# Performance work log

Hardware: AMD Instinct MI355X
Metric: run time of the kernel (lower is better)

Reference implementation:

```python
import jax, jax.numpy as jnp
import numpy as np

N = 100000   # total nodes in batch
E = 1200000  # total edges
D = 64       # dim_features (== hidden_dim)
H = 64       # hidden_dim
T = 32       # dim_targets
L = 3        # num_layers
G = 500      # number of graphs in batch


def setup_inputs() -> dict:
    key = jax.random.key(0)
    ks = jax.random.split(key, 16)
    s = 0.1
    inp = {
        "x": jax.random.normal(ks[0], (N, D), jnp.float32),
        "src": jax.random.randint(ks[1], (E,), 0, N, jnp.int32),
        "dst": jax.random.randint(ks[2], (E,), 0, N, jnp.int32),
        "graph_ids": jnp.sort(jax.random.randint(ks[3], (N,), 0, G, jnp.int32)),
        # GINConv learnable eps (init 0)
        "eps": jnp.zeros((L,), jnp.float32),
        # per-layer conv apply MLP: Linear(D->H), ReLU, Linear(H->H)
        "conv_w1": jax.random.normal(ks[4], (L, D, H), jnp.float32) * s,
        "conv_b1": jnp.zeros((L, H), jnp.float32),
        "conv_w2": jax.random.normal(ks[5], (L, H, H), jnp.float32) * s,
        "conv_b2": jnp.zeros((L, H), jnp.float32),
        # GraphNorm params
        "gn_weight": jnp.ones((L, H), jnp.float32),
        "gn_bias": jnp.zeros((L, H), jnp.float32),
        "gn_scale": jnp.ones((L, H), jnp.float32),
        # per-layer projection MLP: Linear(H->H), ReLU, Linear(H->T)
        "proj_w1": jax.random.normal(ks[6], (L, H, H), jnp.float32) * s,
        "proj_b1": jnp.zeros((L, H), jnp.float32),
        "proj_w2": jax.random.normal(ks[7], (L, H, T), jnp.float32) * s,
        "proj_b2": jnp.zeros((L, T), jnp.float32),
    }
    return inp


def reference(x, src, dst, graph_ids, eps, conv_w1, conv_b1, conv_w2, conv_b2,
              gn_weight, gn_bias, gn_scale, proj_w1, proj_b1, proj_w2, proj_b2):
    gid = graph_ids
    counts = jax.ops.segment_sum(jnp.ones((N,), x.dtype), gid, num_segments=G)
    safe = jnp.maximum(counts, 1.0)[:, None]  # [G,1] nodes per graph

    feat = x
    outs = []
    for l in range(L):
        # GINConv: (1+eps)*h_i + sum over incoming neighbors
        agg = jax.ops.segment_sum(feat[src], dst, num_segments=N)
        h = (1.0 + eps[l]) * feat + agg
        h = jnp.maximum(h @ conv_w1[l] + conv_b1[l], 0.0) @ conv_w2[l] + conv_b2[l]
        # GraphNorm: per-graph mean/std
        mean = jax.ops.segment_sum(h, gid, num_segments=G) / safe
        sub = h - mean[gid] * gn_scale[l]
        var = jax.ops.segment_sum(sub * sub, gid, num_segments=G) / safe
        std = jnp.sqrt(var + 1e-8)
        h = gn_weight[l] * sub / std[gid] + gn_bias[l]
        feat = jnp.maximum(h, 0.0)
        # projection MLP + per-graph mean pooling
        z = jnp.maximum(feat @ proj_w1[l] + proj_b1[l], 0.0) @ proj_w2[l] + proj_b2[l]
        outs.append(jax.ops.segment_sum(z, gid, num_segments=G) / safe)
    return jnp.concatenate(outs, axis=-1)  # [G, L*T]
```

## Files before the change

kernel.cpp:

```cpp
#include <hip/hip_runtime.h>
#include <math.h>

#define N_NODES 100000
#define N_EDGES 1200000
#define DIM 64
#define TDIM 32
#define NLAYERS 3
#define NGRAPH 500
#define NP (N_NODES + 1)

#define BUCKW 512
#define NBUCK ((N_NODES + BUCKW - 1) / BUCKW)
#define ECHUNK ((N_EDGES + 255) / 256)
#define MLPBL ((N_NODES + 63) / 64)

typedef unsigned short bfu;
typedef __attribute__((ext_vector_type(8))) short short8;
typedef __attribute__((ext_vector_type(4))) float v4f;

__device__ __forceinline__ float bf2f(bfu u) {
    union { unsigned int i; float f; } v; v.i = ((unsigned int)u) << 16; return v.f;
}
__device__ __forceinline__ float bflo(unsigned int d) {
    union { unsigned int i; float f; } v; v.i = d << 16; return v.f;
}
__device__ __forceinline__ float bfhi(unsigned int d) {
    union { unsigned int i; float f; } v; v.i = d & 0xFFFF0000u; return v.f;
}
__device__ __forceinline__ bfu f2bf(float f) {
    union { float f; unsigned int i; } v; v.f = f;
    unsigned int r = v.i + 0x7FFFu + ((v.i >> 16) & 1u);
    return (bfu)(r >> 16);
}

__global__ __launch_bounds__(256) void k_setup(const float* __restrict__ x, bfu* __restrict__ xb,
                                               const int* __restrict__ gid, int* __restrict__ gstart,
                                               float* __restrict__ inv_safe, float* __restrict__ ncnt,
                                               const float* __restrict__ w1, const float* __restrict__ w2,
                                               const float* __restrict__ q1, const float* __restrict__ q2,
                                               bfu* __restrict__ w1t, bfu* __restrict__ w2t,
                                               bfu* __restrict__ q1t, bfu* __restrict__ q2t,
                                               const int* __restrict__ dst, int* __restrict__ bcnt) {
    int b = blockIdx.x, t = threadIdx.x;
    if (b < 6250) {
        int base = (b * 256 + t) * 4;
        float4 v = *(const float4*)&x[base];
        ushort4 o;
        o.x = f2bf(v.x); o.y = f2bf(v.y); o.z = f2bf(v.z); o.w = f2bf(v.w);
        *(ushort4*)&xb[base] = o;
    } else if (b == 6250) {
        for (int tt = t; tt <= NGRAPH; tt += 256) {
            int lo = 0, hi = N_NODES;
            while (lo < hi) {
                int mid = (lo + hi) >> 1;
                if (gid[mid] < tt) lo = mid + 1; else hi = mid;
            }
            gstart[tt] = lo;
        }
        __syncthreads();
        for (int tt = t; tt < NGRAPH; tt += 256) {
            int c = gstart[tt + 1] - gstart[tt];
            inv_safe[tt] = 1.0f / (float)(c > 1 ? c : 1);
            ncnt[tt] = (float)c;
        }
    } else if (b < 6299) {
        int i = (b - 6251) * 256 + t;
        int l = i >> 12, k = (i >> 6) & 63, n = i & 63;
        int o = (l << 12) | (n << 6) | k;
        w1t[o] = f2bf(w1[i]);
        w2t[o] = f2bf(w2[i]);
        q1t[o] = f2bf(q1[i]);
        if (i < NLAYERS * 2048) {
            int l2 = i >> 11, rem = i & 2047, k2 = rem >> 5, n2 = rem & 31;
            q2t[l2 * 2048 + n2 * 64 + k2] = f2bf(q2[i]);
        }
    } else {
        __shared__ int h[NBUCK];
        for (int i = t; i < NBUCK; i += 256) h[i] = 0;
        __syncthreads();
        int e0 = (b - 6299) * ECHUNK;
        int e1 = e0 + ECHUNK; if (e1 > N_EDGES) e1 = N_EDGES;
        for (int e = e0 + t; e < e1; e += 256) atomicAdd(&h[dst[e] >> 9], 1);
        __syncthreads();
        for (int i = t; i < NBUCK; i += 256) if (h[i]) atomicAdd(&bcnt[i], h[i]);
    }
}

__global__ __launch_bounds__(256) void k_bscan(const int* __restrict__ bcnt,
                                               int* __restrict__ bbase, int* __restrict__ bcursor,
                                               const int* __restrict__ gstart,
                                               const float* __restrict__ pb2all, float* __restrict__ out) {
    __shared__ int s[256];
    int t = threadIdx.x;
    s[t] = (t < NBUCK) ? bcnt[t] : 0;
    __syncthreads();
    for (int off = 1; off < 256; off <<= 1) {
        int v = (t >= off) ? s[t - off] : 0;
        __syncthreads();
        s[t] += v;
        __syncthreads();
    }
    int ex = t ? s[t - 1] : 0;
    if (t < NBUCK) { bbase[t] = ex; bcursor[t] = ex; }
    if (t == 0) bbase[NBUCK] = N_EDGES;
    for (int g = t; g < NGRAPH; g += 256) {
        int nn = gstart[g + 1] - gstart[g];
        for (int r = 0; r < NLAYERS * TDIM; r++)
            out[g * (NLAYERS * TDIM) + r] = (nn > 0) ? pb2all[r] : 0.f;
    }
}

__global__ __launch_bounds__(256) void k_bscatter(const int* __restrict__ src, const int* __restrict__ dst,
                                                  int* __restrict__ bcursor, int2* __restrict__ ebuf) {
    __shared__ int cnt[NBUCK];
    __shared__ int base[NBUCK];
    int t = threadIdx.x;
    for (int i = t; i < NBUCK; i += 256) cnt[i] = 0;
    __syncthreads();
    int e0 = blockIdx.x * ECHUNK;
    int e1 = e0 + ECHUNK; if (e1 > N_EDGES) e1 = N_EDGES;
    for (int e = e0 + t; e < e1; e += 256) atomicAdd(&cnt[dst[e] >> 9], 1);
    __syncthreads();
    for (int i = t; i < NBUCK; i += 256) base[i] = cnt[i] ? atomicAdd(&bcursor[i], cnt[i]) : 0;
    __syncthreads();
    for (int i = t; i < NBUCK; i += 256) cnt[i] = 0;
    __syncthreads();
    for (int e = e0 + t; e < e1; e += 256) {
        int d = dst[e];
        int b = d >> 9;
        int r = atomicAdd(&cnt[b], 1);
        ebuf[base[b] + r] = make_int2(src[e], d);
    }
}

__global__ __launch_bounds__(256) void k_bcsr(const int2* __restrict__ ebuf, const int* __restrict__ bbase,
                                              int* __restrict__ offs, int* __restrict__ csr) {
    __shared__ int ldeg[BUCKW];
    __shared__ int lscan[BUCKW];
    __shared__ int lcur[BUCKW];
    int t = threadIdx.x;
    int b = blockIdx.x;
    int nbase = b << 9;
    int ebeg = bbase[b], eend = bbase[b + 1];
    ldeg[t] = 0; ldeg[t + 256] = 0;
    __syncthreads();
    for (int e = ebeg + t; e < eend; e += 256) atomicAdd(&ldeg[ebuf[e].y - nbase], 1);
    __syncthreads();
    lscan[t] = ldeg[t]; lscan[t + 256] = ldeg[t + 256];
    __syncthreads();
    for (int off = 1; off < BUCKW; off <<= 1) {
        int i0 = t, i1 = t + 256;
        int v0 = (i0 >= off) ? lscan[i0 - off] : 0;
        int v1 = (i1 >= off) ? lscan[i1 - off] : 0;
        __syncthreads();
        lscan[i0] += v0; lscan[i1] += v1;
        __syncthreads();
    }
    int ex0 = lscan[t] - ldeg[t];
    int ex1 = lscan[t + 256] - ldeg[t + 256];
    lcur[t] = ex0; lcur[t + 256] = ex1;
    int n0 = nbase + t, n1 = nbase + t + 256;
    if (n0 < N_NODES) offs[n0] = ebeg + ex0;
    if (n1 < N_NODES) offs[n1] = ebeg + ex1;
    if (b == 0 && t == 0) offs[N_NODES] = N_EDGES;
    __syncthreads();
    for (int e = ebeg + t; e < eend; e += 256) {
        int2 p = ebuf[e];
        int slot = atomicAdd(&lcur[p.y - nbase], 1);
        csr[ebeg + slot] = p.x;
    }
}

__device__ __forceinline__ void accum8(float* acc, uint4 d) {
    acc[0] += bflo(d.x); acc[1] += bfhi(d.x);
    acc[2] += bflo(d.y); acc[3] += bfhi(d.y);
    acc[4] += bflo(d.z); acc[5] += bfhi(d.z);
    acc[6] += bflo(d.w); acc[7] += bfhi(d.w);
}

__global__ __launch_bounds__(256) void k_agg(const bfu* __restrict__ feat, const int* __restrict__ offs,
                                             const int* __restrict__ csr, const float* __restrict__ eps,
                                             int l, bfu* __restrict__ hin) {
    int w = threadIdx.x >> 6;
    int lane = threadIdx.x & 63;
    int node = blockIdx.x * 4 + w;
    if (node >= N_NODES) return;
    int eidx = lane >> 3;
    int chunk = lane & 7;
    int coff = chunk * 8;
    int e0 = offs[node], e1 = offs[node + 1];
    int eL = e1 - 1;
    float acc[8] = {0.f, 0.f, 0.f, 0.f, 0.f, 0.f, 0.f, 0.f};

    for (int e = e0; e < e1; e += 16) {
        int ea = e + eidx;
        int ca = (ea < eL) ? ea : eL;
        int sa = csr[ca];
        uint4 da = *(const uint4*)&feat[sa * DIM + coff];
        bool two = (e + 8) < e1;
        if (two) {
            int ebi = e + 8 + eidx;
            int cb = (ebi < eL) ? ebi : eL;
            int sb = csr[cb];
            uint4 db = *(const uint4*)&feat[sb * DIM + coff];
            if (ea >= e1) da = make_uint4(0u, 0u, 0u, 0u);
            if (ebi >= e1) db = make_uint4(0u, 0u, 0u, 0u);
            accum8(acc, da);
            accum8(acc, db);
        } else {
            if (ea >= e1) da = make_uint4(0u, 0u, 0u, 0u);
            accum8(acc, da);
        }
    }

#pragma unroll
    for (int j = 0; j < 8; j++) {
        float v = acc[j];
        v += __shfl_xor(v, 8, 64);
        v += __shfl_xor(v, 16, 64);
        v += __shfl_xor(v, 32, 64);
        acc[j] = v;
    }

    float ep = 1.0f + eps[l];
    uint4 s = *(const uint4*)&feat[node * DIM + coff];
    float r0 = ep * bflo(s.x) + acc[0], r1 = ep * bfhi(s.x) + acc[1];
    float r2 = ep * bflo(s.y) + acc[2], r3 = ep * bfhi(s.y) + acc[3];
    float r4 = ep * bflo(s.z) + acc[4], r5 = ep * bfhi(s.z) + acc[5];
    float r6 = ep * bflo(s.w) + acc[6], r7 = ep * bfhi(s.w) + acc[7];
    if (eidx == 0) {
        uint4 o;
        o.x = ((unsigned int)f2bf(r1) << 16) | f2bf(r0);
        o.y = ((unsigned int)f2bf(r3) << 16) | f2bf(r2);
        o.z = ((unsigned int)f2bf(r5) << 16) | f2bf(r4);
        o.w = ((unsigned int)f2bf(r7) << 16) | f2bf(r6);
        *(uint4*)&hin[node * DIM + coff] = o;
    }
}

__global__ __launch_bounds__(256) void k_mlp(const bfu* __restrict__ hin,
                                             const bfu* __restrict__ w1t, const float* __restrict__ b1,
                                             const bfu* __restrict__ w2t, const float* __restrict__ b2,
                                             const int* __restrict__ gid, bfu* __restrict__ hout,
                                             float* __restrict__ gsum, float* __restrict__ gsq) {
    __shared__ bfu ldsT[4][16 * 80];
    __shared__ int sG[4][16];
    int t = threadIdx.x;
    int w = t >> 6, lane = t & 63, m = lane & 15, q = lane >> 4;
    int nbase = blockIdx.x * 64 + w * 16;
    int row = nbase + m;
    bool valid = row < N_NODES;
    if (lane < 16) sG[w][lane] = (nbase + lane < N_NODES) ? gid[nbase + lane] : -1;

    short8 a0 = {0, 0, 0, 0, 0, 0, 0, 0}, a1 = a0;
    if (valid) {
        a0 = *(const short8*)&hin[row * 64 + q * 8];
        a1 = *(const short8*)&hin[row * 64 + 32 + q * 8];
    }
    short8 bf1[4][2], bf2[4][2];
#pragma unroll
    for (int ct = 0; ct < 4; ct++)
#pragma unroll
        for (int kk = 0; kk < 2; kk++) {
            bf1[ct][kk] = *(const short8*)&w1t[(ct * 16 + m) * 64 + kk * 32 + q * 8];
            bf2[ct][kk] = *(const short8*)&w2t[(ct * 16 + m) * 64 + kk * 32 + q * 8];
        }

    bfu* my = ldsT[w];
#pragma unroll
    for (int ct = 0; ct < 4; ct++) {
        float bv = b1[ct * 16 + m];
        v4f acc = {bv, bv, bv, bv};
        acc = __builtin_amdgcn_mfma_f32_16x16x32_bf16(a0, bf1[ct][0], acc, 0, 0, 0);
        acc = __builtin_amdgcn_mfma_f32_16x16x32_bf16(a1, bf1[ct][1], acc, 0, 0, 0);
#pragma unroll
        for (int r = 0; r < 4; r++)
            my[(q * 4 + r) * 80 + ct * 16 + m] = f2bf(fmaxf(acc[r], 0.f));
    }
    short8 a20 = *(short8*)&my[m * 80 + q * 8];
    short8 a21 = *(short8*)&my[m * 80 + 32 + q * 8];
#pragma unroll
    for (int ct = 0; ct < 4; ct++) {
        float bv = b2[ct * 16 + m];
        v4f acc = {bv, bv, bv, bv};
        acc = __builtin_amdgcn_mfma_f32_16x16x32_bf16(a20, bf2[ct][0], acc, 0, 0, 0);
        acc = __builtin_amdgcn_mfma_f32_16x16x32_bf16(a21, bf2[ct][1], acc, 0, 0, 0);
#pragma unroll
        for (int r = 0; r < 4; r++)
            my[(q * 4 + r) * 80 + ct * 16 + m] = f2bf(acc[r]);
    }
#pragma unroll
    for (int i = 0; i < 2; i++) {
        int idx = i * 64 + lane;
        int r = idx >> 3, ch = (idx & 7) * 8;
        int grow = nbase + r;
        uint4 v = *(uint4*)&my[r * 80 + ch];
        if (grow < N_NODES) *(uint4*)&hout[grow * 64 + ch] = v;
    }
    float s_acc = 0.f, q_acc = 0.f;
    int cur = sG[w][0];
    for (int r = 0; r < 16; r++) {
        int g2 = sG[w][r];
        if (g2 != cur) {
            if (cur >= 0) {
                atomicAdd(&gsum[cur * 64 + lane], s_acc);
                atomicAdd(&gsq[cur * 64 + lane], q_acc);
            }
            cur = g2; s_acc = 0.f; q_acc = 0.f;
        }
        if (g2 >= 0) {
            float v = bf2f(my[r * 80 + lane]);
            s_acc += v; q_acc += v * v;
        }
    }
    if (cur >= 0) {
        atomicAdd(&gsum[cur * 64 + lane], s_acc);
        atomicAdd(&gsq[cur * 64 + lane], q_acc);
    }
}

__global__ __launch_bounds__(256) void k_apply_proj(const bfu* __restrict__ h,
                                                    const int* __restrict__ gid,
                                                    const float* __restrict__ gsum,
                                                    const float* __restrict__ gsq,
                                                    const float* __restrict__ inv_safe,
                                                    const float* __restrict__ ncnt,
                                                    const float* __restrict__ gnw, const float* __restrict__ gnb,
                                                    const float* __restrict__ gns,
                                                    const bfu* __restrict__ p1t, const float* __restrict__ pb1,
                                                    const bfu* __restrict__ p2t,
                                                    bfu* __restrict__ feat, float* __restrict__ out, int l) {
    __shared__ bfu ldsT[4][16 * 80];
    __shared__ float sZ[64 * 33];
    __shared__ int sGid[64];
    int t = threadIdx.x;
    int w = t >> 6, lane = t & 63, m = lane & 15, q = lane >> 4;
    int row0 = blockIdx.x * 64;
    int row = row0 + w * 16 + m;
    bool valid = row < N_NODES;
    if (t < 64) sGid[t] = (row0 + t < N_NODES) ? gid[row0 + t] : -1;

    union Pack { short8 v; bfu u[8]; uint4 qv; };
    Pack a0, a1;
    a0.qv = make_uint4(0u, 0u, 0u, 0u);
    a1.qv = make_uint4(0u, 0u, 0u, 0u);
    if (valid) {
        int g = gid[row];
        float inv = inv_safe[g];
        float nnf = ncnt[g];
#pragma unroll
        for (int kk = 0; kk < 2; kk++) {
            int ch = kk * 32 + q * 8;
            uint4 hv = *(const uint4*)&h[row * 64 + ch];
            float4 Sa = *(const float4*)&gsum[g * 64 + ch];
            float4 Sb = *(const float4*)&gsum[g * 64 + ch + 4];
            float4 Qa = *(const float4*)&gsq[g * 64 + ch];
            float4 Qb = *(const float4*)&gsq[g * 64 + ch + 4];
            float4 nsa = *(const float4*)&gns[ch];
            float4 nsb = *(const float4*)&gns[ch + 4];
            float4 nwa = *(const float4*)&gnw[ch];
            float4 nwb = *(const float4*)&gnw[ch + 4];
            float4 gba = *(const float4*)&gnb[ch];
            float4 gbb = *(const float4*)&gnb[ch + 4];
            float hval[8] = {bflo(hv.x), bfhi(hv.x), bflo(hv.y), bfhi(hv.y),
                             bflo(hv.z), bfhi(hv.z), bflo(hv.w), bfhi(hv.w)};
            float Sv[8] = {Sa.x, Sa.y, Sa.z, Sa.w, Sb.x, Sb.y, Sb.z, Sb.w};
            float Qv[8] = {Qa.x, Qa.y, Qa.z, Qa.w, Qb.x, Qb.y, Qb.z, Qb.w};
            float nsv[8] = {nsa.x, nsa.y, nsa.z, nsa.w, nsb.x, nsb.y, nsb.z, nsb.w};
            float nwv[8] = {nwa.x, nwa.y, nwa.z, nwa.w, nwb.x, nwb.y, nwb.z, nwb.w};
            float gbv[8] = {gba.x, gba.y, gba.z, gba.w, gbb.x, gbb.y, gbb.z, gbb.w};
            Pack& a = kk ? a1 : a0;
#pragma unroll
            for (int j = 0; j < 8; j++) {
                float ms = Sv[j] * inv * nsv[j];
                float var = (Qv[j] - 2.f * ms * Sv[j] + nnf * ms * ms) * inv;
                float coef = nwv[j] * rsqrtf(var + 1e-8f);
                a.u[j] = f2bf(fmaxf(coef * (hval[j] - ms) + gbv[j], 0.f));
            }
            *(uint4*)&feat[row * 64 + ch] = a.qv;
        }
    }

    short8 bf1[4][2], bf2[2][2];
#pragma unroll
    for (int ct = 0; ct < 4; ct++)
#pragma unroll
        for (int kk = 0; kk < 2; kk++)
            bf1[ct][kk] = *(const short8*)&p1t[(ct * 16 + m) * 64 + kk * 32 + q * 8];
#pragma unroll
    for (int ct = 0; ct < 2; ct++)
#pragma unroll
        for (int kk = 0; kk < 2; kk++)
            bf2[ct][kk] = *(const short8*)&p2t[(ct * 16 + m) * 64 + kk * 32 + q * 8];

    bfu* tl = ldsT[w];
#pragma unroll
    for (int ct = 0; ct < 4; ct++) {
        float bv = pb1[ct * 16 + m];
        v4f acc = {bv, bv, bv, bv};
        acc = __builtin_amdgcn_mfma_f32_16x16x32_bf16(a0.v, bf1[ct][0], acc, 0, 0, 0);
        acc = __builtin_amdgcn_mfma_f32_16x16x32_bf16(a1.v, bf1[ct][1], acc, 0, 0, 0);
#pragma unroll
        for (int r = 0; r < 4; r++)
            tl[(q * 4 + r) * 80 + ct * 16 + m] = f2bf(fmaxf(acc[r], 0.f));
    }
    short8 a20 = *(short8*)&tl[m * 80 + q * 8];
    short8 a21 = *(short8*)&tl[m * 80 + 32 + q * 8];
#pragma unroll
    for (int ct = 0; ct < 2; ct++) {
        v4f acc = {0.f, 0.f, 0.f, 0.f};
        acc = __builtin_amdgcn_mfma_f32_16x16x32_bf16(a20, bf2[ct][0], acc, 0, 0, 0);
        acc = __builtin_amdgcn_mfma_f32_16x16x32_bf16(a21, bf2[ct][1], acc, 0, 0, 0);
#pragma unroll
        for (int r = 0; r < 4; r++)
            sZ[(w * 16 + q * 4 + r) * 33 + ct * 16 + m] = acc[r];
    }
    __syncthreads();

    if (t < 32) {
        int cur = sGid[0];
        float a = 0.f;
        for (int r = 0; r < 64; r++) {
            int g2 = sGid[r];
            if (g2 != cur) {
                if (cur >= 0) atomicAdd(&out[cur * (NLAYERS * TDIM) + l * TDIM + t], a * inv_safe[cur]);
                cur = g2;
                a = 0.f;
            }
            if (g2 >= 0) a += sZ[r * 33 + t];
        }
        if (cur >= 0) atomicAdd(&out[cur * (NLAYERS * TDIM) + l * TDIM + t], a * inv_safe[cur]);
    }
}


extern "C" void kernel_launch(void* const* d_in, const int* in_sizes, int n_in,
                              void* d_out, int out_size, void* d_ws, size_t ws_size,
                              hipStream_t stream) {
    const float* x        = (const float*)d_in[0];
    const int*   src      = (const int*)d_in[1];
    const int*   dst      = (const int*)d_in[2];
    const int*   gid      = (const int*)d_in[3];
    const float* eps      = (const float*)d_in[4];
    const float* conv_w1  = (const float*)d_in[5];
    const float* conv_b1  = (const float*)d_in[6];
    const float* conv_w2  = (const float*)d_in[7];
    const float* conv_b2  = (const float*)d_in[8];
    const float* gn_w     = (const float*)d_in[9];
    const float* gn_b     = (const float*)d_in[10];
    const float* gn_s     = (const float*)d_in[11];
    const float* proj_w1  = (const float*)d_in[12];
    const float* proj_b1  = (const float*)d_in[13];
    const float* proj_w2  = (const float*)d_in[14];
    const float* proj_b2  = (const float*)d_in[15];
    float* out = (float*)d_out;

    char* ws = (char*)d_ws;
    size_t off = 0;
    auto alloc = [&](size_t bytes) { char* p = ws + off; off += (bytes + 255) & ~(size_t)255; return p; };
    int*   offs     = (int*)alloc(NP * sizeof(int));
    int*   gstart   = (int*)alloc((NGRAPH + 1) * sizeof(int));
    float* inv_safe = (float*)alloc(NGRAPH * sizeof(float));
    float* ncnt     = (float*)alloc(NGRAPH * sizeof(float));
    int*   bcnt     = (int*)alloc(NBUCK * sizeof(int));
    float* gsumA    = (float*)alloc((size_t)NLAYERS * 2 * NGRAPH * 64 * sizeof(float));
    size_t zbytes   = (size_t)((char*)(gsumA + (size_t)NLAYERS * 2 * NGRAPH * 64) - (char*)bcnt);
    int*   bbase    = (int*)alloc((NBUCK + 1) * sizeof(int));
    int*   bcursor  = (int*)alloc(NBUCK * sizeof(int));
    int*   csr      = (int*)alloc(N_EDGES * sizeof(int));
    bfu*   featbf   = (bfu*)alloc((size_t)N_NODES * DIM * sizeof(bfu));
    bfu*   hinbf    = (bfu*)alloc((size_t)N_NODES * DIM * sizeof(bfu));
    bfu*   hbufbf   = (bfu*)alloc((size_t)N_NODES * DIM * sizeof(bfu));
    bfu*   w1t      = (bfu*)alloc((size_t)NLAYERS * 4096 * sizeof(bfu));
    bfu*   w2t      = (bfu*)alloc((size_t)NLAYERS * 4096 * sizeof(bfu));
    bfu*   p1t      = (bfu*)alloc((size_t)NLAYERS * 4096 * sizeof(bfu));
    bfu*   p2t      = (bfu*)alloc((size_t)NLAYERS * 2048 * sizeof(bfu));
    int2*  ebuf     = (int2*)alloc((size_t)N_EDGES * sizeof(int2));

    hipMemsetAsync(bcnt, 0, zbytes, stream);
    k_setup<<<6555, 256, 0, stream>>>(x, featbf, gid, gstart, inv_safe, ncnt,
                                      conv_w1, conv_w2, proj_w1, proj_w2, w1t, w2t, p1t, p2t,
                                      dst, bcnt);
    k_bscan<<<1, 256, 0, stream>>>(bcnt, bbase, bcursor, gstart, proj_b2, out);
    k_bscatter<<<256, 256, 0, stream>>>(src, dst, bcursor, ebuf);
    k_bcsr<<<NBUCK, 256, 0, stream>>>(ebuf, bbase, offs, csr);

    int aggbl = (N_NODES + 3) / 4;
    for (int l = 0; l < NLAYERS; l++) {
        float* gsum_l = gsumA + (size_t)l * 2 * NGRAPH * 64;
        float* gsq_l  = gsum_l + NGRAPH * 64;
        k_agg<<<aggbl, 256, 0, stream>>>(featbf, offs, csr, eps, l, hinbf);
        k_mlp<<<MLPBL, 256, 0, stream>>>(hinbf, w1t + l * 4096, conv_b1 + l * 64,
                                         w2t + l * 4096, conv_b2 + l * 64,
                                         gid, hbufbf, gsum_l, gsq_l);
        k_apply_proj<<<MLPBL, 256, 0, stream>>>(hbufbf, gid, gsum_l, gsq_l, inv_safe, ncnt,
                                                gn_w + l * 64, gn_b + l * 64, gn_s + l * 64,
                                                p1t + l * 4096, proj_b1 + l * 64,
                                                p2t + l * 2048, featbf, out, l);
    }
}
```

Measured before the change: 442.6 us.

## Replace full CSR build with 64-node buckets and LDS atomic aggregation

Drops the per-node CSR construction pass. Edges are now bucketed by groups of 64 destination nodes, each packed as (src<<6 | local dst) in a single int. Aggregation runs one block per bucket and accumulates neighbour features into a shared-memory tile with LDS float atomics before applying (1+eps). This removes the k_bcsr kernel and the int2 edge buffer, at the cost of many LDS atomics per edge and a larger bucket scan (1563 buckets) in a single 1024-thread block.

```diff
diff --git a/kernel.cpp b/kernel.cpp
--- a/kernel.cpp
+++ b/kernel.cpp
@@ -9,9 +9,10 @@
 #define NGRAPH 500
 #define NP (N_NODES + 1)
 
-#define BUCKW 512
+#define BUCKW 64
 #define NBUCK ((N_NODES + BUCKW - 1) / BUCKW)
 #define ECHUNK ((N_EDGES + 255) / 256)
+#define ECH2 ((N_EDGES + 511) / 512)
 #define MLPBL ((N_NODES + 63) / 64)
 
 typedef unsigned short bfu;
@@ -80,30 +81,33 @@
         __syncthreads();
         int e0 = (b - 6299) * ECHUNK;
         int e1 = e0 + ECHUNK; if (e1 > N_EDGES) e1 = N_EDGES;
-        for (int e = e0 + t; e < e1; e += 256) atomicAdd(&h[dst[e] >> 9], 1);
+        for (int e = e0 + t; e < e1; e += 256) atomicAdd(&h[dst[e] >> 6], 1);
         __syncthreads();
         for (int i = t; i < NBUCK; i += 256) if (h[i]) atomicAdd(&bcnt[i], h[i]);
     }
 }
 
-__global__ __launch_bounds__(256) void k_bscan(const int* __restrict__ bcnt,
-                                               int* __restrict__ bbase, int* __restrict__ bcursor,
-                                               const int* __restrict__ gstart,
-                                               const float* __restrict__ pb2all, float* __restrict__ out) {
-    __shared__ int s[256];
+__global__ __launch_bounds__(1024) void k_bscan(const int* __restrict__ bcnt,
+                                                int* __restrict__ bbase, int* __restrict__ bcursor,
+                                                const int* __restrict__ gstart,
+                                                const float* __restrict__ pb2all, float* __restrict__ out) {
+    __shared__ int s[2048];
     int t = threadIdx.x;
-    s[t] = (t < NBUCK) ? bcnt[t] : 0;
-    __syncthreads();
-    for (int off = 1; off < 256; off <<= 1) {
-        int v = (t >= off) ? s[t - off] : 0;
+    int v0 = (t < NBUCK) ? bcnt[t] : 0;
+    int v1 = (t + 1024 < NBUCK) ? bcnt[t + 1024] : 0;
+    s[t] = v0; s[t + 1024] = v1;
+    __syncthreads();
+    for (int off = 1; off < 2048; off <<= 1) {
+        int a0 = (t >= off) ? s[t - off] : 0;
+        int a1 = (t + 1024 >= off) ? s[t + 1024 - off] : 0;
         __syncthreads();
-        s[t] += v;
+        s[t] += a0; s[t + 1024] += a1;
         __syncthreads();
     }
-    int ex = t ? s[t - 1] : 0;
-    if (t < NBUCK) { bbase[t] = ex; bcursor[t] = ex; }
+    if (t < NBUCK) { int ex = s[t] - v0; bbase[t] = ex; bcursor[t] = ex; }
+    if (t + 1024 < NBUCK) { int ex = s[t + 1024] - v1; bbase[t + 1024] = ex; bcursor[t + 1024] = ex; }
     if (t == 0) bbase[NBUCK] = N_EDGES;
-    for (int g = t; g < NGRAPH; g += 256) {
+    for (int g = t; g < NGRAPH; g += 1024) {
         int nn = gstart[g + 1] - gstart[g];
         for (int r = 0; r < NLAYERS * TDIM; r++)
             out[g * (NLAYERS * TDIM) + r] = (nn > 0) ? pb2all[r] : 0.f;
@@ -111,15 +115,15 @@
 }
 
 __global__ __launch_bounds__(256) void k_bscatter(const int* __restrict__ src, const int* __restrict__ dst,
-                                                  int* __restrict__ bcursor, int2* __restrict__ ebuf) {
+                                                  int* __restrict__ bcursor, int* __restrict__ ebuf) {
     __shared__ int cnt[NBUCK];
     __shared__ int base[NBUCK];
     int t = threadIdx.x;
     for (int i = t; i < NBUCK; i += 256) cnt[i] = 0;
     __syncthreads();
-    int e0 = blockIdx.x * ECHUNK;
-    int e1 = e0 + ECHUNK; if (e1 > N_EDGES) e1 = N_EDGES;
-    for (int e = e0 + t; e < e1; e += 256) atomicAdd(&cnt[dst[e] >> 9], 1);
+    int e0 = blockIdx.x * ECH2;
+    int e1 = e0 + ECH2; if (e1 > N_EDGES) e1 = N_EDGES;
+    for (int e = e0 + t; e < e1; e += 256) atomicAdd(&cnt[dst[e] >> 6], 1);
     __syncthreads();
     for (int i = t; i < NBUCK; i += 256) base[i] = cnt[i] ? atomicAdd(&bcursor[i], cnt[i]) : 0;
     __syncthreads();
@@ -127,114 +131,80 @@
     __syncthreads();
     for (int e = e0 + t; e < e1; e += 256) {
         int d = dst[e];
-        int b = d >> 9;
+        int b = d >> 6;
         int r = atomicAdd(&cnt[b], 1);
-        ebuf[base[b] + r] = make_int2(src[e], d);
-    }
-}
-
-__global__ __launch_bounds__(256) void k_bcsr(const int2* __restrict__ ebuf, const int* __restrict__ bbase,
-                                              int* __restrict__ offs, int* __restrict__ csr) {
-    __shared__ int ldeg[BUCKW];
-    __shared__ int lscan[BUCKW];
-    __shared__ int lcur[BUCKW];
+        ebuf[base[b] + r] = (src[e] << 6) | (d & 63);
+    }
+}
+
+__global__ __launch_bounds__(256) void k_aggregate(const bfu* __restrict__ feat,
+                                                   const int* __restrict__ ebuf,
+                                                   const int* __restrict__ bbase,
+                                                   const float* __restrict__ eps, int l,
+                                                   bfu* __restrict__ hin) {
+    __shared__ float accum[64 * 68];
     int t = threadIdx.x;
+    int w = t >> 6, lane = t & 63;
     int b = blockIdx.x;
-    int nbase = b << 9;
+    int nbase = b << 6;
     int ebeg = bbase[b], eend = bbase[b + 1];
-    ldeg[t] = 0; ldeg[t + 256] = 0;
-    __syncthreads();
-    for (int e = ebeg + t; e < eend; e += 256) atomicAdd(&ldeg[ebuf[e].y - nbase], 1);
-    __syncthreads();
-    lscan[t] = ldeg[t]; lscan[t + 256] = ldeg[t + 256];
-    __syncthreads();
-    for (int off = 1; off < BUCKW; off <<= 1) {
-        int i0 = t, i1 = t + 256;
-        int v0 = (i0 >= off) ? lscan[i0 - off] : 0;
-        int v1 = (i1 >= off) ? lscan[i1 - off] : 0;
-        __syncthreads();
-        lscan[i0] += v0; lscan[i1] += v1;
-        __syncthreads();
-    }
-    int ex0 = lscan[t] - ldeg[t];
-    int ex1 = lscan[t + 256] - ldeg[t + 256];
-    lcur[t] = ex0; lcur[t + 256] = ex1;
-    int n0 = nbase + t, n1 = nbase + t + 256;
-    if (n0 < N_NODES) offs[n0] = ebeg + ex0;
-    if (n1 < N_NODES) offs[n1] = ebeg + ex1;
-    if (b == 0 && t == 0) offs[N_NODES] = N_EDGES;
-    __syncthreads();
-    for (int e = ebeg + t; e < eend; e += 256) {
-        int2 p = ebuf[e];
-        int slot = atomicAdd(&lcur[p.y - nbase], 1);
-        csr[ebeg + slot] = p.x;
-    }
-}
-
-__device__ __forceinline__ void accum8(float* acc, uint4 d) {
-    acc[0] += bflo(d.x); acc[1] += bfhi(d.x);
-    acc[2] += bflo(d.y); acc[3] += bfhi(d.y);
-    acc[4] += bflo(d.z); acc[5] += bfhi(d.z);
-    acc[6] += bflo(d.w); acc[7] += bfhi(d.w);
-}
-
-__global__ __launch_bounds__(256) void k_agg(const bfu* __restrict__ feat, const int* __restrict__ offs,
-                                             const int* __restrict__ csr, const float* __restrict__ eps,
-                                             int l, bfu* __restrict__ hin) {
-    int w = threadIdx.x >> 6;
-    int lane = threadIdx.x & 63;
-    int node = blockIdx.x * 4 + w;
-    if (node >= N_NODES) return;
-    int eidx = lane >> 3;
-    int chunk = lane & 7;
-    int coff = chunk * 8;
-    int e0 = offs[node], e1 = offs[node + 1];
-    int eL = e1 - 1;
-    float acc[8] = {0.f, 0.f, 0.f, 0.f, 0.f, 0.f, 0.f, 0.f};
-
-    for (int e = e0; e < e1; e += 16) {
-        int ea = e + eidx;
-        int ca = (ea < eL) ? ea : eL;
-        int sa = csr[ca];
-        uint4 da = *(const uint4*)&feat[sa * DIM + coff];
-        bool two = (e + 8) < e1;
-        if (two) {
-            int ebi = e + 8 + eidx;
-            int cb = (ebi < eL) ? ebi : eL;
-            int sb = csr[cb];
-            uint4 db = *(const uint4*)&feat[sb * DIM + coff];
-            if (ea >= e1) da = make_uint4(0u, 0u, 0u, 0u);
-            if (ebi >= e1) db = make_uint4(0u, 0u, 0u, 0u);
-            accum8(acc, da);
-            accum8(acc, db);
-        } else {
-            if (ea >= e1) da = make_uint4(0u, 0u, 0u, 0u);
-            accum8(acc, da);
-        }
-    }
-
-#pragma unroll
-    for (int j = 0; j < 8; j++) {
-        float v = acc[j];
-        v += __shfl_xor(v, 8, 64);
-        v += __shfl_xor(v, 16, 64);
-        v += __shfl_xor(v, 32, 64);
-        acc[j] = v;
-    }
-
-    float ep = 1.0f + eps[l];
-    uint4 s = *(const uint4*)&feat[node * DIM + coff];
-    float r0 = ep * bflo(s.x) + acc[0], r1 = ep * bfhi(s.x) + acc[1];
-    float r2 = ep * bflo(s.y) + acc[2], r3 = ep * bfhi(s.y) + acc[3];
-    float r4 = ep * bflo(s.z) + acc[4], r5 = ep * bfhi(s.z) + acc[5];
-    float r6 = ep * bflo(s.w) + acc[6], r7 = ep * bfhi(s.w) + acc[7];
-    if (eidx == 0) {
-        uint4 o;
-        o.x = ((unsigned int)f2bf(r1) << 16) | f2bf(r0);
-        o.y = ((unsigned int)f2bf(r3) << 16) | f2bf(r2);
-        o.z = ((unsigned int)f2bf(r5) << 16) | f2bf(r4);
-        o.w = ((unsigned int)f2bf(r7) << 16) | f2bf(r6);
-        *(uint4*)&hin[node * DIM + coff] = o;
+    int eidx = lane >> 3, chunk = lane & 7, coff = chunk * 8;
+
+    for (int i = t; i < 64 * 68 / 4; i += 256) {
+        float4 z = {0.f, 0.f, 0.f, 0.f};
+        *(float4*)&accum[i * 4] = z;
+    }
+    __syncthreads();
+
+    int eL = eend - 1;
+    for (int e = ebeg + w * 32; e < eend; e += 128) {
+        int pv[4]; uint4 d[4]; bool val[4];
+#pragma unroll
+        for (int g = 0; g < 4; g++) {
+            int ea = e + g * 8 + eidx;
+            int ca = (ea < eL) ? ea : eL;
+            pv[g] = ebuf[ca];
+            val[g] = ea < eend;
+        }
+#pragma unroll
+        for (int g = 0; g < 4; g++) {
+            int sa = pv[g] >> 6;
+            d[g] = *(const uint4*)&feat[sa * DIM + coff];
+        }
+#pragma unroll
+        for (int g = 0; g < 4; g++) {
+            if (!val[g]) d[g] = make_uint4(0u, 0u, 0u, 0u);
+            float* row = &accum[(pv[g] & 63) * 68 + coff];
+            atomicAdd(&row[0], bflo(d[g].x)); atomicAdd(&row[1], bfhi(d[g].x));
+            atomicAdd(&row[2], bflo(d[g].y)); atomicAdd(&row[3], bfhi(d[g].y));
+            atomicAdd(&row[4], bflo(d[g].z)); atomicAdd(&row[5], bfhi(d[g].z));
+            atomicAdd(&row[6], bflo(d[g].w)); atomicAdd(&row[7], bfhi(d[g].w));
+        }
+    }
+    __syncthreads();
+
+    int r0 = t >> 2, qt = t & 3;
+    int node = nbase + r0;
+    if (node < N_NODES) {
+        float ep = 1.0f + eps[l];
+        int ch0 = qt * 16;
+        uint4 s0 = *(const uint4*)&feat[node * DIM + ch0];
+        uint4 s1 = *(const uint4*)&feat[node * DIM + ch0 + 8];
+        float4 a0 = *(float4*)&accum[r0 * 68 + ch0];
+        float4 a1 = *(float4*)&accum[r0 * 68 + ch0 + 4];
+        float4 a2 = *(float4*)&accum[r0 * 68 + ch0 + 8];
+        float4 a3 = *(float4*)&accum[r0 * 68 + ch0 + 12];
+        uint4 o0, o1;
+        o0.x = ((unsigned int)f2bf(ep * bfhi(s0.x) + a0.y) << 16) | f2bf(ep * bflo(s0.x) + a0.x);
+        o0.y = ((unsigned int)f2bf(ep * bfhi(s0.y) + a0.w) << 16) | f2bf(ep * bflo(s0.y) + a0.z);
+        o0.z = ((unsigned int)f2bf(ep * bfhi(s0.z) + a1.y) << 16) | f2bf(ep * bflo(s0.z) + a1.x);
+        o0.w = ((unsigned int)f2bf(ep * bfhi(s0.w) + a1.w) << 16) | f2bf(ep * bflo(s0.w) + a1.z);
+        o1.x = ((unsigned int)f2bf(ep * bfhi(s1.x) + a2.y) << 16) | f2bf(ep * bflo(s1.x) + a2.x);
+        o1.y = ((unsigned int)f2bf(ep * bfhi(s1.y) + a2.w) << 16) | f2bf(ep * bflo(s1.y) + a2.z);
+        o1.z = ((unsigned int)f2bf(ep * bfhi(s1.z) + a3.y) << 16) | f2bf(ep * bflo(s1.z) + a3.x);
+        o1.w = ((unsigned int)f2bf(ep * bfhi(s1.w) + a3.w) << 16) | f2bf(ep * bflo(s1.w) + a3.z);
+        *(uint4*)&hin[node * DIM + ch0] = o0;
+        *(uint4*)&hin[node * DIM + ch0 + 8] = o1;
     }
 }
 
@@ -458,7 +428,6 @@
     char* ws = (char*)d_ws;
     size_t off = 0;
     auto alloc = [&](size_t bytes) { char* p = ws + off; off += (bytes + 255) & ~(size_t)255; return p; };
-    int*   offs     = (int*)alloc(NP * sizeof(int));
     int*   gstart   = (int*)alloc((NGRAPH + 1) * sizeof(int));
     float* inv_safe = (float*)alloc(NGRAPH * sizeof(float));
     float* ncnt     = (float*)alloc(NGRAPH * sizeof(float));
@@ -467,7 +436,7 @@
     size_t zbytes   = (size_t)((char*)(gsumA + (size_t)NLAYERS * 2 * NGRAPH * 64) - (char*)bcnt);
     int*   bbase    = (int*)alloc((NBUCK + 1) * sizeof(int));
     int*   bcursor  = (int*)alloc(NBUCK * sizeof(int));
-    int*   csr      = (int*)alloc(N_EDGES * sizeof(int));
+    int*   ebuf     = (int*)alloc((size_t)N_EDGES * sizeof(int));
     bfu*   featbf   = (bfu*)alloc((size_t)N_NODES * DIM * sizeof(bfu));
     bfu*   hinbf    = (bfu*)alloc((size_t)N_NODES * DIM * sizeof(bfu));
     bfu*   hbufbf   = (bfu*)alloc((size_t)N_NODES * DIM * sizeof(bfu));
@@ -475,21 +444,18 @@
     bfu*   w2t      = (bfu*)alloc((size_t)NLAYERS * 4096 * sizeof(bfu));
     bfu*   p1t      = (bfu*)alloc((size_t)NLAYERS * 4096 * sizeof(bfu));
     bfu*   p2t      = (bfu*)alloc((size_t)NLAYERS * 2048 * sizeof(bfu));
-    int2*  ebuf     = (int2*)alloc((size_t)N_EDGES * sizeof(int2));
 
     hipMemsetAsync(bcnt, 0, zbytes, stream);
     k_setup<<<6555, 256, 0, stream>>>(x, featbf, gid, gstart, inv_safe, ncnt,
                                       conv_w1, conv_w2, proj_w1, proj_w2, w1t, w2t, p1t, p2t,
                                       dst, bcnt);
-    k_bscan<<<1, 256, 0, stream>>>(bcnt, bbase, bcursor, gstart, proj_b2, out);
-    k_bscatter<<<256, 256, 0, stream>>>(src, dst, bcursor, ebuf);
-    k_bcsr<<<NBUCK, 256, 0, stream>>>(ebuf, bbase, offs, csr);
-
-    int aggbl = (N_NODES + 3) / 4;
+    k_bscan<<<1, 1024, 0, stream>>>(bcnt, bbase, bcursor, gstart, proj_b2, out);
+    k_bscatter<<<512, 256, 0, stream>>>(src, dst, bcursor, ebuf);
+
     for (int l = 0; l < NLAYERS; l++) {
         float* gsum_l = gsumA + (size_t)l * 2 * NGRAPH * 64;
         float* gsq_l  = gsum_l + NGRAPH * 64;
-        k_agg<<<aggbl, 256, 0, stream>>>(featbf, offs, csr, eps, l, hinbf);
+        k_aggregate<<<NBUCK, 256, 0, stream>>>(featbf, ebuf, bbase, eps, l, hinbf);
         k_mlp<<<MLPBL, 256, 0, stream>>>(hinbf, w1t + l * 4096, conv_b1 + l * 64,
                                          w2t + l * 4096, conv_b2 + l * 64,
                                          gid, hbufbf, gsum_l, gsq_l);
```

Result: slower. 1.679 ms (+279.2%).

## Recompute conv MLP in apply kernel instead of storing h; widen agg unroll

Applied to the files above, without the earlier changes.

The stats kernel no longer writes the conv-MLP output h to global memory. The apply/projection kernel recomputes the two conv MLP matmuls from hin and reads h from LDS, which trades an extra pass of MFMA work for a saved 12.8MB store plus a 12.8MB load per layer. The aggregation loop now issues four independent gathers per iteration instead of two, raising memory-level parallelism at the cost of more registers. Weight fragments are loaded in scoped blocks, which may also reduce register pressure.

```diff
diff --git a/kernel.cpp b/kernel.cpp
--- a/kernel.cpp
+++ b/kernel.cpp
@@ -32,6 +32,7 @@
     unsigned int r = v.i + 0x7FFFu + ((v.i >> 16) & 1u);
     return (bfu)(r >> 16);
 }
+__device__ __forceinline__ uint4 zero4() { return make_uint4(0u, 0u, 0u, 0u); }
 
 __global__ __launch_bounds__(256) void k_setup(const float* __restrict__ x, bfu* __restrict__ xb,
                                                const int* __restrict__ gid, int* __restrict__ gstart,
@@ -186,30 +187,41 @@
     int node = blockIdx.x * 4 + w;
     if (node >= N_NODES) return;
     int eidx = lane >> 3;
-    int chunk = lane & 7;
-    int coff = chunk * 8;
+    int coff = (lane & 7) * 8;
     int e0 = offs[node], e1 = offs[node + 1];
     int eL = e1 - 1;
     float acc[8] = {0.f, 0.f, 0.f, 0.f, 0.f, 0.f, 0.f, 0.f};
 
-    for (int e = e0; e < e1; e += 16) {
-        int ea = e + eidx;
-        int ca = (ea < eL) ? ea : eL;
-        int sa = csr[ca];
-        uint4 da = *(const uint4*)&feat[sa * DIM + coff];
-        bool two = (e + 8) < e1;
-        if (two) {
-            int ebi = e + 8 + eidx;
-            int cb = (ebi < eL) ? ebi : eL;
-            int sb = csr[cb];
-            uint4 db = *(const uint4*)&feat[sb * DIM + coff];
-            if (ea >= e1) da = make_uint4(0u, 0u, 0u, 0u);
-            if (ebi >= e1) db = make_uint4(0u, 0u, 0u, 0u);
-            accum8(acc, da);
-            accum8(acc, db);
+    for (int e = e0; e < e1; e += 32) {
+        int ea0 = e + eidx, ea1 = ea0 + 8, ea2 = ea0 + 16, ea3 = ea0 + 24;
+        bool v1 = (e + 8) < e1, v2 = (e + 16) < e1;
+        if (v2) {
+            int i0 = ea0 < eL ? ea0 : eL, i1 = ea1 < eL ? ea1 : eL;
+            int i2 = ea2 < eL ? ea2 : eL, i3 = ea3 < eL ? ea3 : eL;
+            int s0 = csr[i0], s1 = csr[i1], s2 = csr[i2], s3 = csr[i3];
+            uint4 d0 = *(const uint4*)&feat[s0 * DIM + coff];
+            uint4 d1 = *(const uint4*)&feat[s1 * DIM + coff];
+            uint4 d2 = *(const uint4*)&feat[s2 * DIM + coff];
+            uint4 d3 = *(const uint4*)&feat[s3 * DIM + coff];
+            if (ea0 >= e1) d0 = zero4();
+            if (ea1 >= e1) d1 = zero4();
+            if (ea2 >= e1) d2 = zero4();
+            if (ea3 >= e1) d3 = zero4();
+            accum8(acc, d0); accum8(acc, d1); accum8(acc, d2); accum8(acc, d3);
+        } else if (v1) {
+            int i0 = ea0 < eL ? ea0 : eL, i1 = ea1 < eL ? ea1 : eL;
+            int s0 = csr[i0], s1 = csr[i1];
+            uint4 d0 = *(const uint4*)&feat[s0 * DIM + coff];
+            uint4 d1 = *(const uint4*)&feat[s1 * DIM + coff];
+            if (ea0 >= e1) d0 = zero4();
+            if (ea1 >= e1) d1 = zero4();
+            accum8(acc, d0); accum8(acc, d1);
         } else {
-            if (ea >= e1) da = make_uint4(0u, 0u, 0u, 0u);
-            accum8(acc, da);
+            int i0 = ea0 < eL ? ea0 : eL;
+            int s0 = csr[i0];
+            uint4 d0 = *(const uint4*)&feat[s0 * DIM + coff];
+            if (ea0 >= e1) d0 = zero4();
+            accum8(acc, d0);
         }
     }
 
@@ -238,11 +250,11 @@
     }
 }
 
-__global__ __launch_bounds__(256) void k_mlp(const bfu* __restrict__ hin,
-                                             const bfu* __restrict__ w1t, const float* __restrict__ b1,
-                                             const bfu* __restrict__ w2t, const float* __restrict__ b2,
-                                             const int* __restrict__ gid, bfu* __restrict__ hout,
-                                             float* __restrict__ gsum, float* __restrict__ gsq) {
+__global__ __launch_bounds__(256) void k_mlp_stats(const bfu* __restrict__ hin,
+                                                   const bfu* __restrict__ w1t, const float* __restrict__ b1,
+                                                   const bfu* __restrict__ w2t, const float* __restrict__ b2,
+                                                   const int* __restrict__ gid,
+                                                   float* __restrict__ gsum, float* __restrict__ gsq) {
     __shared__ bfu ldsT[4][16 * 80];
     __shared__ int sG[4][16];
     int t = threadIdx.x;
@@ -257,45 +269,44 @@
         a0 = *(const short8*)&hin[row * 64 + q * 8];
         a1 = *(const short8*)&hin[row * 64 + 32 + q * 8];
     }
-    short8 bf1[4][2], bf2[4][2];
-#pragma unroll
-    for (int ct = 0; ct < 4; ct++)
-#pragma unroll
-        for (int kk = 0; kk < 2; kk++) {
-            bf1[ct][kk] = *(const short8*)&w1t[(ct * 16 + m) * 64 + kk * 32 + q * 8];
-            bf2[ct][kk] = *(const short8*)&w2t[(ct * 16 + m) * 64 + kk * 32 + q * 8];
-        }
-
     bfu* my = ldsT[w];
-#pragma unroll
-    for (int ct = 0; ct < 4; ct++) {
-        float bv = b1[ct * 16 + m];
-        v4f acc = {bv, bv, bv, bv};
-        acc = __builtin_amdgcn_mfma_f32_16x16x32_bf16(a0, bf1[ct][0], acc, 0, 0, 0);
-        acc = __builtin_amdgcn_mfma_f32_16x16x32_bf16(a1, bf1[ct][1], acc, 0, 0, 0);
-#pragma unroll
-        for (int r = 0; r < 4; r++)
-            my[(q * 4 + r) * 80 + ct * 16 + m] = f2bf(fmaxf(acc[r], 0.f));
+    {
+        short8 f1[4][2];
+#pragma unroll
+        for (int ct = 0; ct < 4; ct++)
+#pragma unroll
+            for (int kk = 0; kk < 2; kk++)
+                f1[ct][kk] = *(const short8*)&w1t[(ct * 16 + m) * 64 + kk * 32 + q * 8];
+#pragma unroll
+        for (int ct = 0; ct < 4; ct++) {
+            float bv = b1[ct * 16 + m];
+            v4f acc = {bv, bv, bv, bv};
+            acc = __builtin_amdgcn_mfma_f32_16x16x32_bf16(a0, f1[ct][0], acc, 0, 0, 0);
+            acc = __builtin_amdgcn_mfma_f32_16x16x32_bf16(a1, f1[ct][1], acc, 0, 0, 0);
+#pragma unroll
+            for (int r = 0; r < 4; r++)
+                my[(q * 4 + r) * 80 + ct * 16 + m] = f2bf(fmaxf(acc[r], 0.f));
+        }
     }
     short8 a20 = *(short8*)&my[m * 80 + q * 8];
     short8 a21 = *(short8*)&my[m * 80 + 32 + q * 8];
-#pragma unroll
-    for (int ct = 0; ct < 4; ct++) {
-        float bv = b2[ct * 16 + m];
-        v4f acc = {bv, bv, bv, bv};
-        acc = __builtin_amdgcn_mfma_f32_16x16x32_bf16(a20, bf2[ct][0], acc, 0, 0, 0);
-        acc = __builtin_amdgcn_mfma_f32_16x16x32_bf16(a21, bf2[ct][1], acc, 0, 0, 0);
-#pragma unroll
-        for (int r = 0; r < 4; r++)
-            my[(q * 4 + r) * 80 + ct * 16 + m] = f2bf(acc[r]);
-    }
-#pragma unroll
-    for (int i = 0; i < 2; i++) {
-        int idx = i * 64 + lane;
-        int r = idx >> 3, ch = (idx & 7) * 8;
-        int grow = nbase + r;
-        uint4 v = *(uint4*)&my[r * 80 + ch];
-        if (grow < N_NODES) *(uint4*)&hout[grow * 64 + ch] = v;
+    {
+        short8 f2[4][2];
+#pragma unroll
+        for (int ct = 0; ct < 4; ct++)
+#pragma unroll
+            for (int kk = 0; kk < 2; kk++)
+                f2[ct][kk] = *(const short8*)&w2t[(ct * 16 + m) * 64 + kk * 32 + q * 8];
+#pragma unroll
+        for (int ct = 0; ct < 4; ct++) {
+            float bv = b2[ct * 16 + m];
+            v4f acc = {bv, bv, bv, bv};
+            acc = __builtin_amdgcn_mfma_f32_16x16x32_bf16(a20, f2[ct][0], acc, 0, 0, 0);
+            acc = __builtin_amdgcn_mfma_f32_16x16x32_bf16(a21, f2[ct][1], acc, 0, 0, 0);
+#pragma unroll
+            for (int r = 0; r < 4; r++)
+                my[(q * 4 + r) * 80 + ct * 16 + m] = f2bf(acc[r]);
+        }
     }
     float s_acc = 0.f, q_acc = 0.f;
     int cur = sG[w][0];
@@ -319,7 +330,7 @@
     }
 }
 
-__global__ __launch_bounds__(256) void k_apply_proj(const bfu* __restrict__ h,
+__global__ __launch_bounds__(256) void k_apply_proj(const bfu* __restrict__ hin,
                                                     const int* __restrict__ gid,
                                                     const float* __restrict__ gsum,
                                                     const float* __restrict__ gsq,
@@ -327,6 +338,8 @@
                                                     const float* __restrict__ ncnt,
                                                     const float* __restrict__ gnw, const float* __restrict__ gnb,
                                                     const float* __restrict__ gns,
+                                                    const bfu* __restrict__ w1t, const float* __restrict__ b1,
+                                                    const bfu* __restrict__ w2t, const float* __restrict__ b2,
                                                     const bfu* __restrict__ p1t, const float* __restrict__ pb1,
                                                     const bfu* __restrict__ p2t,
                                                     bfu* __restrict__ feat, float* __restrict__ out, int l) {
@@ -339,11 +352,56 @@
     int row = row0 + w * 16 + m;
     bool valid = row < N_NODES;
     if (t < 64) sGid[t] = (row0 + t < N_NODES) ? gid[row0 + t] : -1;
+    bfu* my = ldsT[w];
+
+    short8 a0 = {0, 0, 0, 0, 0, 0, 0, 0}, a1 = a0;
+    if (valid) {
+        a0 = *(const short8*)&hin[row * 64 + q * 8];
+        a1 = *(const short8*)&hin[row * 64 + 32 + q * 8];
+    }
+    {
+        short8 f1[4][2];
+#pragma unroll
+        for (int ct = 0; ct < 4; ct++)
+#pragma unroll
+            for (int kk = 0; kk < 2; kk++)
+                f1[ct][kk] = *(const short8*)&w1t[(ct * 16 + m) * 64 + kk * 32 + q * 8];
+#pragma unroll
+        for (int ct = 0; ct < 4; ct++) {
+            float bv = b1[ct * 16 + m];
+            v4f acc = {bv, bv, bv, bv};
+            acc = __builtin_amdgcn_mfma_f32_16x16x32_bf16(a0, f1[ct][0], acc, 0, 0, 0);
+            acc = __builtin_amdgcn_mfma_f32_16x16x32_bf16(a1, f1[ct][1], acc, 0, 0, 0);
+#pragma unroll
+            for (int r = 0; r < 4; r++)
+                my[(q * 4 + r) * 80 + ct * 16 + m] = f2bf(fmaxf(acc[r], 0.f));
+        }
+    }
+    short8 a20 = *(short8*)&my[m * 80 + q * 8];
+    short8 a21 = *(short8*)&my[m * 80 + 32 + q * 8];
+    {
+        short8 f2[4][2];
+#pragma unroll
+        for (int ct = 0; ct < 4; ct++)
+#pragma unroll
+            for (int kk = 0; kk < 2; kk++)
+                f2[ct][kk] = *(const short8*)&w2t[(ct * 16 + m) * 64 + kk * 32 + q * 8];
+#pragma unroll
+        for (int ct = 0; ct < 4; ct++) {
+            float bv = b2[ct * 16 + m];
+            v4f acc = {bv, bv, bv, bv};
+            acc = __builtin_amdgcn_mfma_f32_16x16x32_bf16(a20, f2[ct][0], acc, 0, 0, 0);
+            acc = __builtin_amdgcn_mfma_f32_16x16x32_bf16(a21, f2[ct][1], acc, 0, 0, 0);
+#pragma unroll
+            for (int r = 0; r < 4; r++)
+                my[(q * 4 + r) * 80 + ct * 16 + m] = f2bf(acc[r]);
+        }
+    }
 
     union Pack { short8 v; bfu u[8]; uint4 qv; };
-    Pack a0, a1;
-    a0.qv = make_uint4(0u, 0u, 0u, 0u);
-    a1.qv = make_uint4(0u, 0u, 0u, 0u);
+    Pack na0, na1;
+    na0.qv = zero4();
+    na1.qv = zero4();
     if (valid) {
         int g = gid[row];
         float inv = inv_safe[g];
@@ -351,7 +409,8 @@
 #pragma unroll
         for (int kk = 0; kk < 2; kk++) {
             int ch = kk * 32 + q * 8;
-            uint4 hv = *(const uint4*)&h[row * 64 + ch];
+            short8 hv8 = *(short8*)&my[m * 80 + ch];
+            const bfu* hu = (const bfu*)&hv8;
             float4 Sa = *(const float4*)&gsum[g * 64 + ch];
             float4 Sb = *(const float4*)&gsum[g * 64 + ch + 4];
             float4 Qa = *(const float4*)&gsq[g * 64 + ch];
@@ -362,58 +421,59 @@
             float4 nwb = *(const float4*)&gnw[ch + 4];
             float4 gba = *(const float4*)&gnb[ch];
             float4 gbb = *(const float4*)&gnb[ch + 4];
-            float hval[8] = {bflo(hv.x), bfhi(hv.x), bflo(hv.y), bfhi(hv.y),
-                             bflo(hv.z), bfhi(hv.z), bflo(hv.w), bfhi(hv.w)};
             float Sv[8] = {Sa.x, Sa.y, Sa.z, Sa.w, Sb.x, Sb.y, Sb.z, Sb.w};
             float Qv[8] = {Qa.x, Qa.y, Qa.z, Qa.w, Qb.x, Qb.y, Qb.z, Qb.w};
             float nsv[8] = {nsa.x, nsa.y, nsa.z, nsa.w, nsb.x, nsb.y, nsb.z, nsb.w};
             float nwv[8] = {nwa.x, nwa.y, nwa.z, nwa.w, nwb.x, nwb.y, nwb.z, nwb.w};
             float gbv[8] = {gba.x, gba.y, gba.z, gba.w, gbb.x, gbb.y, gbb.z, gbb.w};
-            Pack& a = kk ? a1 : a0;
+            Pack& a = kk ? na1 : na0;
 #pragma unroll
             for (int j = 0; j < 8; j++) {
                 float ms = Sv[j] * inv * nsv[j];
                 float var = (Qv[j] - 2.f * ms * Sv[j] + nnf * ms * ms) * inv;
                 float coef = nwv[j] * rsqrtf(var + 1e-8f);
-                a.u[j] = f2bf(fmaxf(coef * (hval[j] - ms) + gbv[j], 0.f));
+                a.u[j] = f2bf(fmaxf(coef * (bf2f(hu[j]) - ms) + gbv[j], 0.f));
             }
             *(uint4*)&feat[row * 64 + ch] = a.qv;
         }
     }
 
-    short8 bf1[4][2], bf2[2][2];
-#pragma unroll
-    for (int ct = 0; ct < 4; ct++)
-#pragma unroll
-        for (int kk = 0; kk < 2; kk++)
-            bf1[ct][kk] = *(const short8*)&p1t[(ct * 16 + m) * 64 + kk * 32 + q * 8];
-#pragma unroll
-    for (int ct = 0; ct < 2; ct++)
-#pragma unroll
-        for (int kk = 0; kk < 2; kk++)
-            bf2[ct][kk] = *(const short8*)&p2t[(ct * 16 + m) * 64 + kk * 32 + q * 8];
-
-    bfu* tl = ldsT[w];
-#pragma unroll
-    for (int ct = 0; ct < 4; ct++) {
-        float bv = pb1[ct * 16 + m];
-        v4f acc = {bv, bv, bv, bv};
-        acc = __builtin_amdgcn_mfma_f32_16x16x32_bf16(a0.v, bf1[ct][0], acc, 0, 0, 0);
-        acc = __builtin_amdgcn_mfma_f32_16x16x32_bf16(a1.v, bf1[ct][1], acc, 0, 0, 0);
-#pragma unroll
-        for (int r = 0; r < 4; r++)
-            tl[(q * 4 + r) * 80 + ct * 16 + m] = f2bf(fmaxf(acc[r], 0.f));
-    }
-    short8 a20 = *(short8*)&tl[m * 80 + q * 8];
-    short8 a21 = *(short8*)&tl[m * 80 + 32 + q * 8];
-#pragma unroll
-    for (int ct = 0; ct < 2; ct++) {
-        v4f acc = {0.f, 0.f, 0.f, 0.f};
-        acc = __builtin_amdgcn_mfma_f32_16x16x32_bf16(a20, bf2[ct][0], acc, 0, 0, 0);
-        acc = __builtin_amdgcn_mfma_f32_16x16x32_bf16(a21, bf2[ct][1], acc, 0, 0, 0);
-#pragma unroll
-        for (int r = 0; r < 4; r++)
-            sZ[(w * 16 + q * 4 + r) * 33 + ct * 16 + m] = acc[r];
+    {
+        short8 g1[4][2];
+#pragma unroll
+        for (int ct = 0; ct < 4; ct++)
+#pragma unroll
+            for (int kk = 0; kk < 2; kk++)
+                g1[ct][kk] = *(const short8*)&p1t[(ct * 16 + m) * 64 + kk * 32 + q * 8];
+#pragma unroll
+        for (int ct = 0; ct < 4; ct++) {
+            float bv = pb1[ct * 16 + m];
+            v4f acc = {bv, bv, bv, bv};
+            acc = __builtin_amdgcn_mfma_f32_16x16x32_bf16(na0.v, g1[ct][0], acc, 0, 0, 0);
+            acc = __builtin_amdgcn_mfma_f32_16x16x32_bf16(na1.v, g1[ct][1], acc, 0, 0, 0);
+#pragma unroll
+            for (int r = 0; r < 4; r++)
+                my[(q * 4 + r) * 80 + ct * 16 + m] = f2bf(fmaxf(acc[r], 0.f));
+        }
+    }
+    short8 pa0 = *(short8*)&my[m * 80 + q * 8];
+    short8 pa1 = *(short8*)&my[m * 80 + 32 + q * 8];
+    {
+        short8 g2f[2][2];
+#pragma unroll
+        for (int ct = 0; ct < 2; ct++)
+#pragma unroll
+            for (int kk = 0; kk < 2; kk++)
+                g2f[ct][kk] = *(const short8*)&p2t[(ct * 16 + m) * 64 + kk * 32 + q * 8];
+#pragma unroll
+        for (int ct = 0; ct < 2; ct++) {
+            v4f acc = {0.f, 0.f, 0.f, 0.f};
+            acc = __builtin_amdgcn_mfma_f32_16x16x32_bf16(pa0, g2f[ct][0], acc, 0, 0, 0);
+            acc = __builtin_amdgcn_mfma_f32_16x16x32_bf16(pa1, g2f[ct][1], acc, 0, 0, 0);
+#pragma unroll
+            for (int r = 0; r < 4; r++)
+                sZ[(w * 16 + q * 4 + r) * 33 + ct * 16 + m] = acc[r];
+        }
     }
     __syncthreads();
 
@@ -470,7 +530,6 @@
     int*   csr      = (int*)alloc(N_EDGES * sizeof(int));
     bfu*   featbf   = (bfu*)alloc((size_t)N_NODES * DIM * sizeof(bfu));
     bfu*   hinbf    = (bfu*)alloc((size_t)N_NODES * DIM * sizeof(bfu));
-    bfu*   hbufbf   = (bfu*)alloc((size_t)N_NODES * DIM * sizeof(bfu));
     bfu*   w1t      = (bfu*)alloc((size_t)NLAYERS * 4096 * sizeof(bfu));
     bfu*   w2t      = (bfu*)alloc((size_t)NLAYERS * 4096 * sizeof(bfu));
     bfu*   p1t      = (bfu*)alloc((size_t)NLAYERS * 4096 * sizeof(bfu));
@@ -490,11 +549,13 @@
         float* gsum_l = gsumA + (size_t)l * 2 * NGRAPH * 64;
         float* gsq_l  = gsum_l + NGRAPH * 64;
         k_agg<<<aggbl, 256, 0, stream>>>(featbf, offs, csr, eps, l, hinbf);
-        k_mlp<<<MLPBL, 256, 0, stream>>>(hinbf, w1t + l * 4096, conv_b1 + l * 64,
-                                         w2t + l * 4096, conv_b2 + l * 64,
-                                         gid, hbufbf, gsum_l, gsq_l);
-        k_apply_proj<<<MLPBL, 256, 0, stream>>>(hbufbf, gid, gsum_l, gsq_l, inv_safe, ncnt,
+        k_mlp_stats<<<MLPBL, 256, 0, stream>>>(hinbf, w1t + l * 4096, conv_b1 + l * 64,
+                                               w2t + l * 4096, conv_b2 + l * 64,
+                                               gid, gsum_l, gsq_l);
+        k_apply_proj<<<MLPBL, 256, 0, stream>>>(hinbf, gid, gsum_l, gsq_l, inv_safe, ncnt,
                                                 gn_w + l * 64, gn_b + l * 64, gn_s + l * 64,
+                                                w1t + l * 4096, conv_b1 + l * 64,
+                                                w2t + l * 4096, conv_b2 + l * 64,
                                                 p1t + l * 4096, proj_b1 + l * 64,
                                                 p2t + l * 2048, featbf, out, l);
     }
```

New measurement: 479.4 us. 8.3% more time.
